# Optimization experiments

Measured on AMD Instinct MI355X. Metric: run time of the kernel, lower is better.

## Reference

```python
import jax, jax.numpy as jnp
import numpy as np

N, V, J, NB = 512, 3889, 35, 20
PARENTS = np.array([0, 0, 1, 2, 3, 4, 5, 6, 7, 8, 9, 6, 11, 12, 13, 6, 15, 16, 17, 18,
                    16, 20, 21, 22, 23, 16, 25, 26, 27, 28, 29, 30, 16, 1, 1], dtype=np.int32)


def _rodrigues(theta):
    # theta: [M,3] axis-angle -> [M,3,3] rotation matrices (batch_rodrigues)
    angle = jnp.sqrt(jnp.sum(theta * theta, axis=1, keepdims=True) + 1e-8)  # [M,1]
    r = theta / angle                                                        # [M,3]
    c = jnp.cos(angle)[..., None]                                            # [M,1,1]
    s = jnp.sin(angle)[..., None]
    rr = r[:, :, None] * r[:, None, :]                                       # [M,3,3]
    z = jnp.zeros_like(r[:, 0])
    K = jnp.stack([z, -r[:, 2], r[:, 1],
                   r[:, 2], z, -r[:, 0],
                   -r[:, 1], r[:, 0], z], axis=1).reshape(-1, 3, 3)
    eye = jnp.eye(3, dtype=theta.dtype)
    return c * eye + (1.0 - c) * rr + s * K


def _make_A(R, t):
    # R: [N,3,3], t: [N,3] -> homogeneous [N,4,4]
    n = R.shape[0]
    top = jnp.concatenate([R, t[:, :, None]], axis=2)                        # [N,3,4]
    bot = jnp.broadcast_to(jnp.array([0.0, 0.0, 0.0, 1.0], R.dtype), (n, 1, 4))
    return jnp.concatenate([top, bot], axis=1)


def _global_rigid(Rs, Jp, scales, parents):
    # Rs: [N,35,3,3], Jp: [N,35,3], scales: [N,35,3] (diag scale factors)
    # diag(s_par)^-1 @ R @ diag(s) == R * s[col] / s_par[row]
    results = [_make_A(Rs[:, 0], Jp[:, 0])]
    for i in range(1, len(parents)):  # fixed 35-joint kinematic tree
        p = int(parents[i])
        j_here = Jp[:, i] - Jp[:, p]
        rot_new = Rs[:, i] * (scales[:, i][:, None, :] / scales[:, p][:, :, None])
        results.append(results[p] @ _make_A(rot_new, j_here))
    results = jnp.stack(results, axis=1)                                     # [N,35,4,4]
    new_J = results[:, :, :3, 3]
    # A = results - pad(results @ [J;0]) : subtract rest-pose bone from last column
    init_bone = jnp.einsum('njab,njb->nja', results[:, :, :, :3], Jp)        # [N,35,4]
    A = results - jnp.pad(init_bone[..., None], ((0, 0), (0, 0), (0, 0), (3, 0)))
    return new_J, A


def reference(beta, theta, betas_extra, deform_verts, trans, v_template,
              shapedirs, posedirs, J_regressor, weights, parents):
    par = np.asarray(jax.device_get(parents))
    n = beta.shape[0]
    v_shaped = v_template + deform_verts + (beta @ shapedirs).reshape(n, V, 3)
    Jp = jnp.einsum('nvc,vj->njc', v_shaped, J_regressor)                    # [N,35,3]
    Rs = _rodrigues(theta.reshape(n * J, 3)).reshape(n, J, 3, 3)
    pose_feature = (Rs[:, 1:] - jnp.eye(3, dtype=Rs.dtype)).reshape(n, 306)
    v_posed = (pose_feature @ posedirs).reshape(n, V, 3) + v_shaped
    scales = betas_extra.reshape(n, J, 3)
    _, A = _global_rigid(Rs, Jp, scales, par)
    T = jnp.einsum('vj,njab->nvab', weights, A)                              # [N,V,4,4] LBS blend
    v_h = jnp.concatenate([v_posed, jnp.ones((n, V, 1), v_posed.dtype)], axis=2)
    verts = jnp.einsum('nvab,nvb->nva', T, v_h)[..., :3] + trans[:, None, :]
    joints = jnp.einsum('nvc,vj->njc', verts, J_regressor)
    return verts, joints, Rs


def setup_inputs() -> dict:
    key = jax.random.key(0)
    ks = jax.random.split(key, 10)
    beta = 0.5 * jax.random.normal(ks[0], (N, NB), jnp.float32)
    theta = 0.2 * jax.random.normal(ks[1], (N, J * 3), jnp.float32)
    betas_extra = jnp.exp(0.1 * jax.random.normal(ks[2], (N, J * 3), jnp.float32))  # positive scales ~1
    deform_verts = 0.01 * jax.random.normal(ks[3], (N, V, 3), jnp.float32)
    trans = jax.random.normal(ks[4], (N, 3), jnp.float32)
    v_template = jax.random.normal(ks[5], (V, 3), jnp.float32)
    shapedirs = 0.01 * jax.random.normal(ks[6], (NB, V * 3), jnp.float32)
    posedirs = 0.01 * jax.random.normal(ks[7], (306, V * 3), jnp.float32)
    Jr = jax.random.uniform(ks[8], (V, J), jnp.float32)
    J_regressor = Jr / jnp.sum(Jr, axis=0, keepdims=True)   # columns sum to 1
    Wt = jax.random.uniform(ks[9], (V, J), jnp.float32)
    weights = Wt / jnp.sum(Wt, axis=1, keepdims=True)       # rows sum to 1 (skinning weights)
    return {"beta": beta, "theta": theta, "betas_extra": betas_extra,
            "deform_verts": deform_verts, "trans": trans, "v_template": v_template,
            "shapedirs": shapedirs, "posedirs": posedirs, "J_regressor": J_regressor,
            "weights": weights, "parents": jnp.asarray(PARENTS)}
```

## Files before the change

### kernel.cpp

```cpp
#include <hip/hip_runtime.h>

#define N_   512
#define V_   3889
#define V3   11667
#define J_   35
#define NB_  20
#define PF_K 306
#define KP2  352
#define KS2  11
#define EP2  11776
#define WROWS 3920
#define VP   3904
#define JRROWS 36

typedef __attribute__((ext_vector_type(8))) short short8;
typedef __attribute__((ext_vector_type(4))) float f32x4;

__constant__ int c_parents[J_] = {0,0,1,2,3,4,5,6,7,8,9,6,11,12,13,6,15,16,17,18,
                                  16,20,21,22,23,16,25,26,27,28,29,30,16,1,1};

static __device__ __forceinline__ unsigned short f2bf(float x) {
  union { float f; unsigned int u; } v; v.f = x;
  unsigned int r = v.u + 0x7FFF + ((v.u >> 16) & 1);
  return (unsigned short)(r >> 16);
}

#define PA_JRT 549
#define PA_WTS 245
#define PA_PD  2024
#define PA_BLOCKS (PA_JRT + PA_WTS + PA_PD)
__global__ __launch_bounds__(256) void k_prep_a(
    const float* __restrict__ Jr,  const float* __restrict__ wts,
    const float* __restrict__ pd,  const float* __restrict__ sd,
    float* __restrict__ JrT, unsigned short* __restrict__ wtsB,
    unsigned short* __restrict__ pdT) {
  int b = blockIdx.x;
  int t = threadIdx.x;
  if (b < PA_JRT) {
    int idx = b * 256 + t;
    if (idx >= JRROWS * VP) return;
    int j = idx / VP, v = idx - j * VP;
    JrT[idx] = (j < J_ && v < V_) ? Jr[v * J_ + j] : 0.f;
  } else if (b < PA_JRT + PA_WTS) {
    int bb = b - PA_JRT;
    int v   = bb * 16 + (t >> 4);
    int jk0 = (t & 15) * 4;
    unsigned short pk[4];
#pragma unroll
    for (int i = 0; i < 4; ++i) {
      int j = jk0 + i;
      float x = (v < V_ && j < J_) ? wts[(size_t)v * J_ + j] : 0.f;
      pk[i] = f2bf(x);
    }
    *(unsigned long long*)(wtsB + (size_t)v * 64 + jk0) = *(unsigned long long*)pk;
  } else {
    int pp = b - (PA_JRT + PA_WTS);
    int ec = pp % 184, o4 = pp / 184;
    int e  = ec * 64 + (t & 63);
    int oc = o4 * 4 + (t >> 6);
    int k0 = oc * 8;
    bool ev = e < V3;
    union { unsigned short u[8]; short8 s; } pk;
#pragma unroll
    for (int ii = 0; ii < 8; ++ii) {
      int k = k0 + ii;
      float x = 0.f;
      if (ev && k < PF_K)            x = pd[(size_t)k * V3 + e];
      else if (ev && k < PF_K + NB_) x = sd[(size_t)(k - PF_K) * V3 + e];
      pk.u[ii] = f2bf(x);
    }
    *(short8*)(pdT + (size_t)e * KP2 + k0) = pk.s;
  }
}

#define JRJG 9
__global__ __launch_bounds__(512) void k_jp_plus(
    const float* __restrict__ deform, const float* __restrict__ JrT,
    const float* __restrict__ vt,     const float* __restrict__ sd,
    float* __restrict__ JpRaw, float* __restrict__ vtsdJr) {
  __shared__ float part[8][27];
  int b = blockIdx.x;
  int t = threadIdx.x;
  int lane = t & 63, w = t >> 6;
  int jg = w & 3, vh = w >> 2;
  int j0 = jg * JRJG;

  const float* s0;
  int c0, cn;
  bool tail;
  if (b < N_) {
    s0 = deform + (size_t)b * V3;
    c0 = vh ? 8 : 0; cn = vh ? 7 : 8; tail = (vh == 1);
  } else {
    int bb = b - N_;
    int d = bb >> 2, ch = bb & 3;
    s0 = (d == 0) ? vt : sd + (size_t)(d - 1) * V3;
    c0 = ch * 4 + vh * 2; cn = 2; tail = false;
    if (ch == 3 && vh == 1) { cn = 1; tail = true; }
  }

  const float* jrb = JrT + (size_t)j0 * VP;
  float acc[JRJG][3];
#pragma unroll
  for (int jj = 0; jj < JRJG; ++jj)
#pragma unroll
    for (int cc = 0; cc < 3; ++cc) acc[jj][cc] = 0.f;

  for (int i = 0; i < cn; ++i) {
    int v = (c0 + i) * 256 + lane * 4;
    f32x4 jr4[JRJG];
#pragma unroll
    for (int jj = 0; jj < JRJG; ++jj)
      jr4[jj] = *(const f32x4*)&jrb[(size_t)jj * VP + v];
    const float* dp = s0 + 3 * v;
    f32x4 da = *(const f32x4*)(dp);
    f32x4 db = *(const f32x4*)(dp + 4);
    f32x4 dc = *(const f32x4*)(dp + 8);
#pragma unroll
    for (int jj = 0; jj < JRJG; ++jj) {
      acc[jj][0] += jr4[jj][0]*da[0] + jr4[jj][1]*da[3] + jr4[jj][2]*db[2] + jr4[jj][3]*dc[1];
      acc[jj][1] += jr4[jj][0]*da[1] + jr4[jj][1]*db[0] + jr4[jj][2]*db[3] + jr4[jj][3]*dc[2];
      acc[jj][2] += jr4[jj][0]*da[2] + jr4[jj][1]*db[1] + jr4[jj][2]*dc[0] + jr4[jj][3]*dc[3];
    }
  }

  if (tail) {
    int v = 15 * 256 + lane * 4;
#pragma unroll
    for (int k = 0; k < 4; ++k) {
      int vv = v + k;
      if (vv < V_) {
        float dx = s0[3*vv], dy = s0[3*vv+1], dz = s0[3*vv+2];
#pragma unroll
        for (int jj = 0; jj < JRJG; ++jj) {
          float jr = jrb[(size_t)jj * VP + vv];
          acc[jj][0] += jr * dx; acc[jj][1] += jr * dy; acc[jj][2] += jr * dz;
        }
      }
    }
  }

#pragma unroll
  for (int jj = 0; jj < JRJG; ++jj)
#pragma unroll
    for (int cc = 0; cc < 3; ++cc) {
      float v = acc[jj][cc];
#pragma unroll
      for (int off = 32; off > 0; off >>= 1)
        v += __shfl_down(v, off, 64);
      if (lane == 0) part[w][jj * 3 + cc] = v;
    }
  __syncthreads();

  if (t < 108) {
    int g = t / 27, idx = t % 27;
    int j = g * JRJG + idx / 3;
    if (j < J_) {
      float val = part[g][idx] + part[g + 4][idx];
      if (b < N_) JpRaw[b * 105 + j * 3 + idx % 3] = val;
      else atomicAdd(&vtsdJr[((b - N_) >> 2) * 105 + j * 3 + idx % 3], val);
    }
  }
}

__global__ __launch_bounds__(512) void k_jreduce5(
    const float* __restrict__ src, const float* __restrict__ JrT,
    float* __restrict__ dst) {
  __shared__ float part[8][27];
  int t = threadIdx.x;
  int lane = t & 63;
  int w = t >> 6;
  int jg = w & 3, vh = w >> 2;
  int n = blockIdx.x;
  int j0 = jg * JRJG;
  const float* s0 = src + (size_t)n * V3;
  const float* jrb = JrT + (size_t)j0 * VP;

  int c0 = vh ? 8 : 0;
  int cn = vh ? 7 : 8;
  bool tail = (vh == 1);

  float acc[JRJG][3];
#pragma unroll
  for (int jj = 0; jj < JRJG; ++jj)
#pragma unroll
    for (int cc = 0; cc < 3; ++cc) acc[jj][cc] = 0.f;

  for (int i = 0; i < cn; ++i) {
    int v = (c0 + i) * 256 + lane * 4;
    f32x4 jr4[JRJG];
#pragma unroll
    for (int jj = 0; jj < JRJG; ++jj)
      jr4[jj] = *(const f32x4*)&jrb[(size_t)jj * VP + v];
    const float* dp = s0 + 3 * v;
    f32x4 da = *(const f32x4*)(dp);
    f32x4 db = *(const f32x4*)(dp + 4);
    f32x4 dc = *(const f32x4*)(dp + 8);
#pragma unroll
    for (int jj = 0; jj < JRJG; ++jj) {
      acc[jj][0] += jr4[jj][0]*da[0] + jr4[jj][1]*da[3] + jr4[jj][2]*db[2] + jr4[jj][3]*dc[1];
      acc[jj][1] += jr4[jj][0]*da[1] + jr4[jj][1]*db[0] + jr4[jj][2]*db[3] + jr4[jj][3]*dc[2];
      acc[jj][2] += jr4[jj][0]*da[2] + jr4[jj][1]*db[1] + jr4[jj][2]*dc[0] + jr4[jj][3]*dc[3];
    }
  }

  if (tail) {
    int v = 15 * 256 + lane * 4;
#pragma unroll
    for (int k = 0; k < 4; ++k) {
      int vv = v + k;
      if (vv < V_) {
        float dx = s0[3*vv], dy = s0[3*vv+1], dz = s0[3*vv+2];
#pragma unroll
        for (int jj = 0; jj < JRJG; ++jj) {
          float jr = jrb[(size_t)jj * VP + vv];
          acc[jj][0] += jr * dx; acc[jj][1] += jr * dy; acc[jj][2] += jr * dz;
        }
      }
    }
  }

#pragma unroll
  for (int jj = 0; jj < JRJG; ++jj)
#pragma unroll
    for (int cc = 0; cc < 3; ++cc) {
      float v = acc[jj][cc];
#pragma unroll
      for (int off = 32; off > 0; off >>= 1)
        v += __shfl_down(v, off, 64);
      if (lane == 0) part[w][jj * 3 + cc] = v;
    }
  __syncthreads();

  if (t < 108) {
    int g = t / 27, idx = t % 27;
    int j = g * JRJG + idx / 3;
    if (j < J_)
      dst[n * 105 + j * 3 + idx % 3] = part[g][idx] + part[g + 4][idx];
  }
}

__global__ __launch_bounds__(256) void k_chain_rod(
    const float* __restrict__ theta, const float* __restrict__ JpRaw,
    const float* __restrict__ vtsdJr,
    const float* __restrict__ se,    const float* __restrict__ trans,
    const float* __restrict__ beta,
    float* __restrict__ Rs_out, unsigned short* __restrict__ pfA,
    unsigned short* __restrict__ AwB) {
  __shared__ float loc[4][J_][12];
  __shared__ float res[4][J_][12];
  __shared__ float Jp_s[4][J_][3];
  int t = threadIdx.x;
  int w = t >> 6, l = t & 63;
  int n = blockIdx.x * 4 + w;
  int mt = n >> 4, m = n & 15;

  float r[9];
  if (l < J_) {
    int j = l;
    const float* th = theta + n * (J_ * 3) + j * 3;
    float t0 = th[0], t1 = th[1], t2 = th[2];
    float angle = sqrtf(t0 * t0 + t1 * t1 + t2 * t2 + 1e-8f);
    float inv = 1.0f / angle;
    float r0 = t0 * inv, r1 = t1 * inv, r2 = t2 * inv;
    float s, c;
    sincosf(angle, &s, &c);
    float omc = 1.0f - c;
    r[0] = c + omc * r0 * r0;      r[1] = omc * r0 * r1 - s * r2;  r[2] = omc * r0 * r2 + s * r1;
    r[3] = omc * r1 * r0 + s * r2; r[4] = c + omc * r1 * r1;       r[5] = omc * r1 * r2 - s * r0;
    r[6] = omc * r2 * r0 - s * r1; r[7] = omc * r2 * r1 + s * r0;  r[8] = c + omc * r2 * r2;

    float* ro = Rs_out + (size_t)n * (J_ * 9) + j * 9;
#pragma unroll
    for (int k = 0; k < 9; ++k) ro[k] = r[k];
    if (j > 0) {
#pragma unroll
      for (int kk = 0; kk < 9; ++kk) {
        int k = (j - 1) * 9 + kk;
        float v = r[kk] - ((kk == 0 || kk == 4 || kk == 8) ? 1.0f : 0.0f);
        size_t idx = ((((size_t)mt * KS2 + (k >> 5)) * 4 + ((k >> 3) & 3)) * 16 + m) * 8 + (k & 7);
        pfA[idx] = f2bf(v);
      }
    }
    const float* bn = beta + n * NB_;
#pragma unroll
    for (int cc = 0; cc < 3; ++cc) {
      int jc = j * 3 + cc;
      float val = JpRaw[n * 105 + jc] + vtsdJr[jc];
#pragma unroll
      for (int bb = 0; bb < NB_; ++bb)
        val += bn[bb] * vtsdJr[(1 + bb) * 105 + jc];
      Jp_s[w][j][cc] = val;
    }
  } else {
    unsigned short* An = AwB + (size_t)n * 16 * 64 + l;
#pragma unroll
    for (int d = 0; d < 16; ++d) An[d * 64] = 0;
    if (l < 55) {
      int k = PF_K + (l - 35);
      size_t idx = ((((size_t)mt * KS2 + (k >> 5)) * 4 + ((k >> 3) & 3)) * 16 + m) * 8 + (k & 7);
      pfA[idx] = f2bf(beta[n * NB_ + (l - 35)]);
    } else {
      for (int k = PF_K + NB_ + (l - 55); k < KP2; k += 9) {
        size_t idx = ((((size_t)mt * KS2 + (k >> 5)) * 4 + ((k >> 3) & 3)) * 16 + m) * 8 + (k & 7);
        pfA[idx] = 0;
      }
    }
  }
  __syncthreads();

  if (l < J_) {
    int j = l;
    if (j == 0) {
#pragma unroll
      for (int rr = 0; rr < 3; ++rr) {
        loc[w][0][rr * 4 + 0] = r[rr * 3 + 0];
        loc[w][0][rr * 4 + 1] = r[rr * 3 + 1];
        loc[w][0][rr * 4 + 2] = r[rr * 3 + 2];
        loc[w][0][rr * 4 + 3] = Jp_s[w][0][rr];
      }
#pragma unroll
      for (int k = 0; k < 12; ++k) res[w][0][k] = loc[w][0][k];
    } else {
      int p = c_parents[j];
      float si[3], sp[3], jh[3];
#pragma unroll
      for (int cidx = 0; cidx < 3; ++cidx) {
        si[cidx] = se[n * 105 + j * 3 + cidx];
        sp[cidx] = se[n * 105 + p * 3 + cidx];
        jh[cidx] = Jp_s[w][j][cidx] - Jp_s[w][p][cidx];
      }
#pragma unroll
      for (int rr = 0; rr < 3; ++rr) {
        float invp = 1.0f / sp[rr];
        loc[w][j][rr * 4 + 0] = r[rr * 3 + 0] * si[0] * invp;
        loc[w][j][rr * 4 + 1] = r[rr * 3 + 1] * si[1] * invp;
        loc[w][j][rr * 4 + 2] = r[rr * 3 + 2] * si[2] * invp;
        loc[w][j][rr * 4 + 3] = jh[rr];
      }
    }
  }
  __syncthreads();

  for (int i = 1; i < J_; ++i) {
    if (l < 12) {
      int p = c_parents[i];
      int rr = l >> 2, cc = l & 3;
      float acc = (cc == 3) ? res[w][p][rr * 4 + 3] : 0.f;
#pragma unroll
      for (int k = 0; k < 3; ++k)
        acc += res[w][p][rr * 4 + k] * loc[w][i][k * 4 + cc];
      res[w][i][l] = acc;
    }
    __syncthreads();
  }

  if (l < J_) {
    int j = l;
    float jx = Jp_s[w][j][0];
    float jy = Jp_s[w][j][1];
    float jz = Jp_s[w][j][2];
    unsigned short* An = AwB + (size_t)n * 16 * 64 + j;
#pragma unroll
    for (int rr = 0; rr < 3; ++rr) {
      float a0 = res[w][j][rr * 4 + 0];
      float a1 = res[w][j][rr * 4 + 1];
      float a2 = res[w][j][rr * 4 + 2];
      float a3 = res[w][j][rr * 4 + 3] - (a0 * jx + a1 * jy + a2 * jz)
               + trans[n * 3 + rr];
      An[(rr * 4 + 0) * 64] = f2bf(a0);
      An[(rr * 4 + 1) * 64] = f2bf(a1);
      An[(rr * 4 + 2) * 64] = f2bf(a2);
      An[(rr * 4 + 3) * 64] = f2bf(a3);
    }
  }
}

#define LSTR 242
__global__ __launch_bounds__(256) void k_vposed_skin(
    const unsigned short* __restrict__ pfA, const unsigned short* __restrict__ pdT,
    const unsigned short* __restrict__ AwB, const unsigned short* __restrict__ wtsB,
    const float* __restrict__ vt, const float* __restrict__ deform,
    float* __restrict__ verts) {
  __shared__ float lds[64 * LSTR];
  int t = threadIdx.x;
  int wv = t >> 6, lane = t & 63;
  int q = lane >> 4, col = lane & 15;
  int bx = blockIdx.x, by = blockIdx.y;
  int mtg0 = by * 4;
  int ebase = bx * 240 + wv * 64;

  const short8* Ap = (const short8*)pfA;
  const short8* Bp = (const short8*)pdT;

  f32x4 acc[4][4];
#pragma unroll
  for (int mt = 0; mt < 4; ++mt)
#pragma unroll
    for (int et = 0; et < 4; ++et) acc[mt][et] = (f32x4){0.f, 0.f, 0.f, 0.f};

#pragma unroll
  for (int ks = 0; ks < KS2; ++ks) {
    short8 a[4];
#pragma unroll
    for (int mt = 0; mt < 4; ++mt)
      a[mt] = Ap[(((mtg0 + mt) * KS2 + ks) * 4 + q) * 16 + col];
    short8 b[4];
#pragma unroll
    for (int et = 0; et < 4; ++et)
      b[et] = Bp[(size_t)(ebase + et * 16 + col) * (KP2 / 8) + ks * 4 + q];
#pragma unroll
    for (int mt = 0; mt < 4; ++mt)
#pragma unroll
      for (int et = 0; et < 4; ++et)
        acc[mt][et] = __builtin_amdgcn_mfma_f32_16x16x32_bf16(a[mt], b[et], acc[mt][et], 0, 0, 0);
  }

#pragma unroll
  for (int et = 0; et < 4; ++et) {
    int e_loc = wv * 64 + et * 16 + col;
    int e = bx * 240 + e_loc;
    bool ev = (e < V3) && (e_loc < 240);
    float vte = ev ? vt[e] : 0.f;
#pragma unroll
    for (int mt = 0; mt < 4; ++mt) {
#pragma unroll
      for (int r = 0; r < 4; ++r) {
        int n_loc = mt * 16 + q * 4 + r;
        if (ev) {
          int n = by * 64 + n_loc;
          float df = deform[(size_t)n * V3 + e];
          lds[n_loc * LSTR + e_loc] = acc[mt][et][r] + vte + df;
        }
      }
    }
  }
  __syncthreads();

  short8 bw0[5], bw1[5];
#pragma unroll
  for (int v5 = 0; v5 < 5; ++v5) {
    int v = bx * 80 + v5 * 16 + col;
    const short8* Wp = (const short8*)(wtsB + (size_t)v * 64);
    bw0[v5] = Wp[q];
    bw1[v5] = Wp[4 + q];
  }
#pragma unroll 2
  for (int ni = 0; ni < 16; ++ni) {
    int n_loc = wv * 16 + ni;
    int n = by * 64 + n_loc;
    const short8* Aq = (const short8*)(AwB + ((size_t)n * 16 + col) * 64);
    short8 a0 = Aq[q];
    short8 a1 = Aq[4 + q];
#pragma unroll
    for (int v5 = 0; v5 < 5; ++v5) {
      f32x4 s = (f32x4){0.f, 0.f, 0.f, 0.f};
      s = __builtin_amdgcn_mfma_f32_16x16x32_bf16(a0, bw0[v5], s, 0, 0, 0);
      s = __builtin_amdgcn_mfma_f32_16x16x32_bf16(a1, bw1[v5], s, 0, 0, 0);
      int vl = v5 * 16 + col;
      int v = bx * 80 + vl;
      if (v < V_ && q < 3) {
        float x = lds[n_loc * LSTR + 3 * vl + 0];
        float y = lds[n_loc * LSTR + 3 * vl + 1];
        float z = lds[n_loc * LSTR + 3 * vl + 2];
        verts[(size_t)n * V3 + 3 * v + q] = s[0] * x + s[1] * y + s[2] * z + s[3];
      }
    }
  }
}

extern "C" void kernel_launch(void* const* d_in, const int* in_sizes, int n_in,
                              void* d_out, int out_size, void* d_ws, size_t ws_size,
                              hipStream_t stream) {
  const float* beta   = (const float*)d_in[0];
  const float* theta  = (const float*)d_in[1];
  const float* se     = (const float*)d_in[2];
  const float* deform = (const float*)d_in[3];
  const float* trans  = (const float*)d_in[4];
  const float* vt     = (const float*)d_in[5];
  const float* sd     = (const float*)d_in[6];
  const float* pd     = (const float*)d_in[7];
  const float* Jr     = (const float*)d_in[8];
  const float* wts    = (const float*)d_in[9];

  float* out    = (float*)d_out;
  float* verts  = out;
  float* joints = out + (size_t)N_ * V3;
  float* Rs     = joints + (size_t)N_ * 105;

  char* w = (char*)d_ws;
  unsigned short* pdT    = (unsigned short*)w;
  unsigned short* pfA    = (unsigned short*)(w + 8290304);
  float* JpRaw  = (float*)(w + 8650752);
  unsigned short* AwB    = (unsigned short*)(w + 8865792);
  float* JrT    = (float*)(w + 9914368);
  unsigned short* wtsB   = (unsigned short*)(w + 10476544);
  float* vtsdJr = (float*)(w + 10978304);

  hipMemsetAsync(vtsdJr, 0, 21 * 105 * sizeof(float), stream);
  k_prep_a<<<PA_BLOCKS, 256, 0, stream>>>(Jr, wts, pd, sd, JrT, wtsB, pdT);
  k_jp_plus<<<N_ + 84, 512, 0, stream>>>(deform, JrT, vt, sd, JpRaw, vtsdJr);
  k_chain_rod<<<N_ / 4, 256, 0, stream>>>(theta, JpRaw, vtsdJr, se, trans, beta,
                                          Rs, pfA, AwB);
  k_vposed_skin<<<dim3(49, 8), 256, 0, stream>>>(pfA, pdT, AwB, wtsB, vt, deform, verts);
  k_jreduce5<<<N_, 512, 0, stream>>>(verts, JrT, joints);
}
```

Measured before the change: 209.4 us.

## Process four batch items per block in joint-regressor reductions to reuse JrT loads

Both joint-regression kernels now handle four batch samples per block instead of one, loading each J_regressor tile once and applying it to four deform or vertex rows. This cuts repeated JrT global and L2 traffic by a factor of four and shrinks the grid from 512 to 128 blocks. The cost is four times more accumulator registers per thread (108 floats), which can lower occupancy or cause spills, and fewer blocks may underfill the 256 CUs.

```diff
diff --git a/kernel.cpp b/kernel.cpp
--- a/kernel.cpp
+++ b/kernel.cpp
@@ -12,6 +12,7 @@
 #define WROWS 3920
 #define VP   3904
 #define JRROWS 36
+#define NBLK 128
 
 typedef __attribute__((ext_vector_type(8))) short short8;
 typedef __attribute__((ext_vector_type(4))) float f32x4;
@@ -78,165 +79,257 @@
     const float* __restrict__ deform, const float* __restrict__ JrT,
     const float* __restrict__ vt,     const float* __restrict__ sd,
     float* __restrict__ JpRaw, float* __restrict__ vtsdJr) {
-  __shared__ float part[8][27];
+  __shared__ float part[8][108];
   int b = blockIdx.x;
   int t = threadIdx.x;
   int lane = t & 63, w = t >> 6;
   int jg = w & 3, vh = w >> 2;
   int j0 = jg * JRJG;
-
-  const float* s0;
-  int c0, cn;
-  bool tail;
-  if (b < N_) {
-    s0 = deform + (size_t)b * V3;
-    c0 = vh ? 8 : 0; cn = vh ? 7 : 8; tail = (vh == 1);
+  const float* jrb = JrT + (size_t)j0 * VP;
+
+  if (b < NBLK) {
+    int n0 = b * 4;
+    float acc[4][JRJG][3];
+#pragma unroll
+    for (int nn = 0; nn < 4; ++nn)
+#pragma unroll
+      for (int jj = 0; jj < JRJG; ++jj)
+#pragma unroll
+        for (int cc = 0; cc < 3; ++cc) acc[nn][jj][cc] = 0.f;
+
+    int c0 = vh ? 8 : 0;
+    int cn = vh ? 7 : 8;
+    for (int i = 0; i < cn; ++i) {
+      int v = (c0 + i) * 256 + lane * 4;
+      f32x4 jr4[JRJG];
+#pragma unroll
+      for (int jj = 0; jj < JRJG; ++jj)
+        jr4[jj] = *(const f32x4*)&jrb[(size_t)jj * VP + v];
+#pragma unroll
+      for (int nn = 0; nn < 4; ++nn) {
+        const float* dp = deform + (size_t)(n0 + nn) * V3 + 3 * v;
+        f32x4 da = *(const f32x4*)(dp);
+        f32x4 db = *(const f32x4*)(dp + 4);
+        f32x4 dc = *(const f32x4*)(dp + 8);
+#pragma unroll
+        for (int jj = 0; jj < JRJG; ++jj) {
+          acc[nn][jj][0] += jr4[jj][0]*da[0] + jr4[jj][1]*da[3] + jr4[jj][2]*db[2] + jr4[jj][3]*dc[1];
+          acc[nn][jj][1] += jr4[jj][0]*da[1] + jr4[jj][1]*db[0] + jr4[jj][2]*db[3] + jr4[jj][3]*dc[2];
+          acc[nn][jj][2] += jr4[jj][0]*da[2] + jr4[jj][1]*db[1] + jr4[jj][2]*dc[0] + jr4[jj][3]*dc[3];
+        }
+      }
+    }
+
+    if (vh == 1) {
+      int v = 15 * 256 + lane * 4;
+#pragma unroll
+      for (int k = 0; k < 4; ++k) {
+        int vv = v + k;
+        if (vv < V_) {
+          float jr[JRJG];
+#pragma unroll
+          for (int jj = 0; jj < JRJG; ++jj)
+            jr[jj] = jrb[(size_t)jj * VP + vv];
+#pragma unroll
+          for (int nn = 0; nn < 4; ++nn) {
+            const float* dp = deform + (size_t)(n0 + nn) * V3 + 3 * vv;
+            float dx = dp[0], dy = dp[1], dz = dp[2];
+#pragma unroll
+            for (int jj = 0; jj < JRJG; ++jj) {
+              acc[nn][jj][0] += jr[jj] * dx;
+              acc[nn][jj][1] += jr[jj] * dy;
+              acc[nn][jj][2] += jr[jj] * dz;
+            }
+          }
+        }
+      }
+    }
+
+#pragma unroll
+    for (int nn = 0; nn < 4; ++nn)
+#pragma unroll
+      for (int jj = 0; jj < JRJG; ++jj)
+#pragma unroll
+        for (int cc = 0; cc < 3; ++cc) {
+          float v = acc[nn][jj][cc];
+#pragma unroll
+          for (int off = 32; off > 0; off >>= 1)
+            v += __shfl_down(v, off, 64);
+          if (lane == 0) part[w][nn * 27 + jj * 3 + cc] = v;
+        }
+    __syncthreads();
+
+    if (t < 108) {
+      int g = t / 27, idx = t % 27;
+      int j = g * JRJG + idx / 3;
+      if (j < J_) {
+#pragma unroll
+        for (int nn = 0; nn < 4; ++nn)
+          JpRaw[(n0 + nn) * 105 + j * 3 + idx % 3] =
+              part[g][nn * 27 + idx] + part[g + 4][nn * 27 + idx];
+      }
+    }
   } else {
-    int bb = b - N_;
+    int bb = b - NBLK;
     int d = bb >> 2, ch = bb & 3;
-    s0 = (d == 0) ? vt : sd + (size_t)(d - 1) * V3;
-    c0 = ch * 4 + vh * 2; cn = 2; tail = false;
+    const float* s0 = (d == 0) ? vt : sd + (size_t)(d - 1) * V3;
+    int c0 = ch * 4 + vh * 2, cn = 2;
+    bool tail = false;
     if (ch == 3 && vh == 1) { cn = 1; tail = true; }
-  }
-
+
+    float acc[JRJG][3];
+#pragma unroll
+    for (int jj = 0; jj < JRJG; ++jj)
+#pragma unroll
+      for (int cc = 0; cc < 3; ++cc) acc[jj][cc] = 0.f;
+
+    for (int i = 0; i < cn; ++i) {
+      int v = (c0 + i) * 256 + lane * 4;
+      f32x4 jr4[JRJG];
+#pragma unroll
+      for (int jj = 0; jj < JRJG; ++jj)
+        jr4[jj] = *(const f32x4*)&jrb[(size_t)jj * VP + v];
+      const float* dp = s0 + 3 * v;
+      f32x4 da = *(const f32x4*)(dp);
+      f32x4 db = *(const f32x4*)(dp + 4);
+      f32x4 dc = *(const f32x4*)(dp + 8);
+#pragma unroll
+      for (int jj = 0; jj < JRJG; ++jj) {
+        acc[jj][0] += jr4[jj][0]*da[0] + jr4[jj][1]*da[3] + jr4[jj][2]*db[2] + jr4[jj][3]*dc[1];
+        acc[jj][1] += jr4[jj][0]*da[1] + jr4[jj][1]*db[0] + jr4[jj][2]*db[3] + jr4[jj][3]*dc[2];
+        acc[jj][2] += jr4[jj][0]*da[2] + jr4[jj][1]*db[1] + jr4[jj][2]*dc[0] + jr4[jj][3]*dc[3];
+      }
+    }
+
+    if (tail) {
+      int v = 15 * 256 + lane * 4;
+#pragma unroll
+      for (int k = 0; k < 4; ++k) {
+        int vv = v + k;
+        if (vv < V_) {
+          float dx = s0[3*vv], dy = s0[3*vv+1], dz = s0[3*vv+2];
+#pragma unroll
+          for (int jj = 0; jj < JRJG; ++jj) {
+            float jr = jrb[(size_t)jj * VP + vv];
+            acc[jj][0] += jr * dx; acc[jj][1] += jr * dy; acc[jj][2] += jr * dz;
+          }
+        }
+      }
+    }
+
+#pragma unroll
+    for (int jj = 0; jj < JRJG; ++jj)
+#pragma unroll
+      for (int cc = 0; cc < 3; ++cc) {
+        float v = acc[jj][cc];
+#pragma unroll
+        for (int off = 32; off > 0; off >>= 1)
+          v += __shfl_down(v, off, 64);
+        if (lane == 0) part[w][jj * 3 + cc] = v;
+      }
+    __syncthreads();
+
+    if (t < 108) {
+      int g = t / 27, idx = t % 27;
+      int j = g * JRJG + idx / 3;
+      if (j < J_)
+        atomicAdd(&vtsdJr[(bb >> 2) * 105 + j * 3 + idx % 3],
+                  part[g][idx] + part[g + 4][idx]);
+    }
+  }
+}
+
+__global__ __launch_bounds__(512) void k_jreduce5(
+    const float* __restrict__ src, const float* __restrict__ JrT,
+    float* __restrict__ dst) {
+  __shared__ float part[8][108];
+  int t = threadIdx.x;
+  int lane = t & 63;
+  int w = t >> 6;
+  int jg = w & 3, vh = w >> 2;
+  int n0 = blockIdx.x * 4;
+  int j0 = jg * JRJG;
   const float* jrb = JrT + (size_t)j0 * VP;
-  float acc[JRJG][3];
-#pragma unroll
-  for (int jj = 0; jj < JRJG; ++jj)
-#pragma unroll
-    for (int cc = 0; cc < 3; ++cc) acc[jj][cc] = 0.f;
-
+
+  float acc[4][JRJG][3];
+#pragma unroll
+  for (int nn = 0; nn < 4; ++nn)
+#pragma unroll
+    for (int jj = 0; jj < JRJG; ++jj)
+#pragma unroll
+      for (int cc = 0; cc < 3; ++cc) acc[nn][jj][cc] = 0.f;
+
+  int c0 = vh ? 8 : 0;
+  int cn = vh ? 7 : 8;
   for (int i = 0; i < cn; ++i) {
     int v = (c0 + i) * 256 + lane * 4;
     f32x4 jr4[JRJG];
 #pragma unroll
     for (int jj = 0; jj < JRJG; ++jj)
       jr4[jj] = *(const f32x4*)&jrb[(size_t)jj * VP + v];
-    const float* dp = s0 + 3 * v;
-    f32x4 da = *(const f32x4*)(dp);
-    f32x4 db = *(const f32x4*)(dp + 4);
-    f32x4 dc = *(const f32x4*)(dp + 8);
-#pragma unroll
-    for (int jj = 0; jj < JRJG; ++jj) {
-      acc[jj][0] += jr4[jj][0]*da[0] + jr4[jj][1]*da[3] + jr4[jj][2]*db[2] + jr4[jj][3]*dc[1];
-      acc[jj][1] += jr4[jj][0]*da[1] + jr4[jj][1]*db[0] + jr4[jj][2]*db[3] + jr4[jj][3]*dc[2];
-      acc[jj][2] += jr4[jj][0]*da[2] + jr4[jj][1]*db[1] + jr4[jj][2]*dc[0] + jr4[jj][3]*dc[3];
-    }
-  }
-
-  if (tail) {
+#pragma unroll
+    for (int nn = 0; nn < 4; ++nn) {
+      const float* dp = src + (size_t)(n0 + nn) * V3 + 3 * v;
+      f32x4 da = *(const f32x4*)(dp);
+      f32x4 db = *(const f32x4*)(dp + 4);
+      f32x4 dc = *(const f32x4*)(dp + 8);
+#pragma unroll
+      for (int jj = 0; jj < JRJG; ++jj) {
+        acc[nn][jj][0] += jr4[jj][0]*da[0] + jr4[jj][1]*da[3] + jr4[jj][2]*db[2] + jr4[jj][3]*dc[1];
+        acc[nn][jj][1] += jr4[jj][0]*da[1] + jr4[jj][1]*db[0] + jr4[jj][2]*db[3] + jr4[jj][3]*dc[2];
+        acc[nn][jj][2] += jr4[jj][0]*da[2] + jr4[jj][1]*db[1] + jr4[jj][2]*dc[0] + jr4[jj][3]*dc[3];
+      }
+    }
+  }
+
+  if (vh == 1) {
     int v = 15 * 256 + lane * 4;
 #pragma unroll
     for (int k = 0; k < 4; ++k) {
       int vv = v + k;
       if (vv < V_) {
-        float dx = s0[3*vv], dy = s0[3*vv+1], dz = s0[3*vv+2];
-#pragma unroll
-        for (int jj = 0; jj < JRJG; ++jj) {
-          float jr = jrb[(size_t)jj * VP + vv];
-          acc[jj][0] += jr * dx; acc[jj][1] += jr * dy; acc[jj][2] += jr * dz;
+        float jr[JRJG];
+#pragma unroll
+        for (int jj = 0; jj < JRJG; ++jj)
+          jr[jj] = jrb[(size_t)jj * VP + vv];
+#pragma unroll
+        for (int nn = 0; nn < 4; ++nn) {
+          const float* dp = src + (size_t)(n0 + nn) * V3 + 3 * vv;
+          float dx = dp[0], dy = dp[1], dz = dp[2];
+#pragma unroll
+          for (int jj = 0; jj < JRJG; ++jj) {
+            acc[nn][jj][0] += jr[jj] * dx;
+            acc[nn][jj][1] += jr[jj] * dy;
+            acc[nn][jj][2] += jr[jj] * dz;
+          }
         }
       }
     }
   }
 
 #pragma unroll
-  for (int jj = 0; jj < JRJG; ++jj)
-#pragma unroll
-    for (int cc = 0; cc < 3; ++cc) {
-      float v = acc[jj][cc];
-#pragma unroll
-      for (int off = 32; off > 0; off >>= 1)
-        v += __shfl_down(v, off, 64);
-      if (lane == 0) part[w][jj * 3 + cc] = v;
-    }
+  for (int nn = 0; nn < 4; ++nn)
+#pragma unroll
+    for (int jj = 0; jj < JRJG; ++jj)
+#pragma unroll
+      for (int cc = 0; cc < 3; ++cc) {
+        float v = acc[nn][jj][cc];
+#pragma unroll
+        for (int off = 32; off > 0; off >>= 1)
+          v += __shfl_down(v, off, 64);
+        if (lane == 0) part[w][nn * 27 + jj * 3 + cc] = v;
+      }
   __syncthreads();
 
   if (t < 108) {
     int g = t / 27, idx = t % 27;
     int j = g * JRJG + idx / 3;
     if (j < J_) {
-      float val = part[g][idx] + part[g + 4][idx];
-      if (b < N_) JpRaw[b * 105 + j * 3 + idx % 3] = val;
-      else atomicAdd(&vtsdJr[((b - N_) >> 2) * 105 + j * 3 + idx % 3], val);
-    }
-  }
-}
-
-__global__ __launch_bounds__(512) void k_jreduce5(
-    const float* __restrict__ src, const float* __restrict__ JrT,
-    float* __restrict__ dst) {
-  __shared__ float part[8][27];
-  int t = threadIdx.x;
-  int lane = t & 63;
-  int w = t >> 6;
-  int jg = w & 3, vh = w >> 2;
-  int n = blockIdx.x;
-  int j0 = jg * JRJG;
-  const float* s0 = src + (size_t)n * V3;
-  const float* jrb = JrT + (size_t)j0 * VP;
-
-  int c0 = vh ? 8 : 0;
-  int cn = vh ? 7 : 8;
-  bool tail = (vh == 1);
-
-  float acc[JRJG][3];
-#pragma unroll
-  for (int jj = 0; jj < JRJG; ++jj)
-#pragma unroll
-    for (int cc = 0; cc < 3; ++cc) acc[jj][cc] = 0.f;
-
-  for (int i = 0; i < cn; ++i) {
-    int v = (c0 + i) * 256 + lane * 4;
-    f32x4 jr4[JRJG];
-#pragma unroll
-    for (int jj = 0; jj < JRJG; ++jj)
-      jr4[jj] = *(const f32x4*)&jrb[(size_t)jj * VP + v];
-    const float* dp = s0 + 3 * v;
-    f32x4 da = *(const f32x4*)(dp);
-    f32x4 db = *(const f32x4*)(dp + 4);
-    f32x4 dc = *(const f32x4*)(dp + 8);
-#pragma unroll
-    for (int jj = 0; jj < JRJG; ++jj) {
-      acc[jj][0] += jr4[jj][0]*da[0] + jr4[jj][1]*da[3] + jr4[jj][2]*db[2] + jr4[jj][3]*dc[1];
-      acc[jj][1] += jr4[jj][0]*da[1] + jr4[jj][1]*db[0] + jr4[jj][2]*db[3] + jr4[jj][3]*dc[2];
-      acc[jj][2] += jr4[jj][0]*da[2] + jr4[jj][1]*db[1] + jr4[jj][2]*dc[0] + jr4[jj][3]*dc[3];
-    }
-  }
-
-  if (tail) {
-    int v = 15 * 256 + lane * 4;
-#pragma unroll
-    for (int k = 0; k < 4; ++k) {
-      int vv = v + k;
-      if (vv < V_) {
-        float dx = s0[3*vv], dy = s0[3*vv+1], dz = s0[3*vv+2];
-#pragma unroll
-        for (int jj = 0; jj < JRJG; ++jj) {
-          float jr = jrb[(size_t)jj * VP + vv];
-          acc[jj][0] += jr * dx; acc[jj][1] += jr * dy; acc[jj][2] += jr * dz;
-        }
-      }
-    }
-  }
-
-#pragma unroll
-  for (int jj = 0; jj < JRJG; ++jj)
-#pragma unroll
-    for (int cc = 0; cc < 3; ++cc) {
-      float v = acc[jj][cc];
-#pragma unroll
-      for (int off = 32; off > 0; off >>= 1)
-        v += __shfl_down(v, off, 64);
-      if (lane == 0) part[w][jj * 3 + cc] = v;
-    }
-  __syncthreads();
-
-  if (t < 108) {
-    int g = t / 27, idx = t % 27;
-    int j = g * JRJG + idx / 3;
-    if (j < J_)
-      dst[n * 105 + j * 3 + idx % 3] = part[g][idx] + part[g + 4][idx];
+#pragma unroll
+      for (int nn = 0; nn < 4; ++nn)
+        dst[(n0 + nn) * 105 + j * 3 + idx % 3] =
+            part[g][nn * 27 + idx] + part[g + 4][nn * 27 + idx];
+    }
   }
 }
 
@@ -499,9 +592,9 @@
 
   hipMemsetAsync(vtsdJr, 0, 21 * 105 * sizeof(float), stream);
   k_prep_a<<<PA_BLOCKS, 256, 0, stream>>>(Jr, wts, pd, sd, JrT, wtsB, pdT);
-  k_jp_plus<<<N_ + 84, 512, 0, stream>>>(deform, JrT, vt, sd, JpRaw, vtsdJr);
+  k_jp_plus<<<NBLK + 84, 512, 0, stream>>>(deform, JrT, vt, sd, JpRaw, vtsdJr);
   k_chain_rod<<<N_ / 4, 256, 0, stream>>>(theta, JpRaw, vtsdJr, se, trans, beta,
                                           Rs, pfA, AwB);
   k_vposed_skin<<<dim3(49, 8), 256, 0, stream>>>(pfA, pdT, AwB, wtsB, vt, deform, verts);
-  k_jreduce5<<<N_, 512, 0, stream>>>(verts, JrT, joints);
+  k_jreduce5<<<NBLK, 512, 0, stream>>>(verts, JrT, joints);
 }
```

Result: slower. 256.5 us (+22.5%).

## Replace FP32 joint-regressor reductions with bf16 MFMA GEMM over expanded regressor

Applied to the files above, without the earlier changes.

Builds a bf16 expanded joint regressor (105 x 11776, zero-padded per coordinate) in the prep kernel. Both per-batch joint regressions, over deform and over the final verts, now run as split-K 16x16x32 bf16 MFMA GEMMs that write partial planes. The planes are summed in chain_rod and in a new fold kernel. This trades the scalar FP32 dot-product kernels for matrix cores, at the cost of bf16 rounding of vertices, extra planes traffic, more prep work and one more launch.

```diff
diff --git a/kernel.cpp b/kernel.cpp
--- a/kernel.cpp
+++ b/kernel.cpp
@@ -9,9 +9,12 @@
 #define KP2  352
 #define KS2  11
 #define EP2  11776
-#define WROWS 3920
 #define VP   3904
 #define JRROWS 36
+#define JCP  112
+#define KB_  23
+#define ECH  512
+#define PLN  57344
 
 typedef __attribute__((ext_vector_type(8))) short short8;
 typedef __attribute__((ext_vector_type(4))) float f32x4;
@@ -28,12 +31,13 @@
 #define PA_JRT 549
 #define PA_WTS 245
 #define PA_PD  2024
-#define PA_BLOCKS (PA_JRT + PA_WTS + PA_PD)
+#define PA_JB  644
+#define PA_BLOCKS (PA_JRT + PA_WTS + PA_PD + PA_JB)
 __global__ __launch_bounds__(256) void k_prep_a(
     const float* __restrict__ Jr,  const float* __restrict__ wts,
     const float* __restrict__ pd,  const float* __restrict__ sd,
     float* __restrict__ JrT, unsigned short* __restrict__ wtsB,
-    unsigned short* __restrict__ pdT) {
+    unsigned short* __restrict__ pdT, unsigned short* __restrict__ JrBigT) {
   int b = blockIdx.x;
   int t = threadIdx.x;
   if (b < PA_JRT) {
@@ -53,7 +57,7 @@
       pk[i] = f2bf(x);
     }
     *(unsigned long long*)(wtsB + (size_t)v * 64 + jk0) = *(unsigned long long*)pk;
-  } else {
+  } else if (b < PA_JRT + PA_WTS + PA_PD) {
     int pp = b - (PA_JRT + PA_WTS);
     int ec = pp % 184, o4 = pp / 184;
     int e  = ec * 64 + (t & 63);
@@ -70,36 +74,41 @@
       pk.u[ii] = f2bf(x);
     }
     *(short8*)(pdT + (size_t)e * KP2 + k0) = pk.s;
+  } else {
+    int o = (b - (PA_JRT + PA_WTS + PA_PD)) * 256 + t;
+    int jc = o / 1472;
+    int eo = (o - jc * 1472) * 8;
+    int jj = jc / 3, cc = jc - jj * 3;
+    union { unsigned short u[8]; short8 s; } pk;
+#pragma unroll
+    for (int i = 0; i < 8; ++i) {
+      int e = eo + i;
+      int v = e / 3, ce = e - v * 3;
+      float x = (jc < 105 && e < V3 && ce == cc) ? Jr[v * J_ + jj] : 0.f;
+      pk.u[i] = f2bf(x);
+    }
+    *(short8*)(JrBigT + (size_t)jc * EP2 + eo) = pk.s;
   }
 }
 
 #define JRJG 9
-__global__ __launch_bounds__(512) void k_jp_plus(
-    const float* __restrict__ deform, const float* __restrict__ JrT,
-    const float* __restrict__ vt,     const float* __restrict__ sd,
-    float* __restrict__ JpRaw, float* __restrict__ vtsdJr) {
+__global__ __launch_bounds__(512) void k_jp84(
+    const float* __restrict__ JrT, const float* __restrict__ vt,
+    const float* __restrict__ sd,  float* __restrict__ vtsdJr) {
   __shared__ float part[8][27];
   int b = blockIdx.x;
   int t = threadIdx.x;
   int lane = t & 63, w = t >> 6;
   int jg = w & 3, vh = w >> 2;
   int j0 = jg * JRJG;
-
-  const float* s0;
-  int c0, cn;
-  bool tail;
-  if (b < N_) {
-    s0 = deform + (size_t)b * V3;
-    c0 = vh ? 8 : 0; cn = vh ? 7 : 8; tail = (vh == 1);
-  } else {
-    int bb = b - N_;
-    int d = bb >> 2, ch = bb & 3;
-    s0 = (d == 0) ? vt : sd + (size_t)(d - 1) * V3;
-    c0 = ch * 4 + vh * 2; cn = 2; tail = false;
-    if (ch == 3 && vh == 1) { cn = 1; tail = true; }
-  }
-
   const float* jrb = JrT + (size_t)j0 * VP;
+
+  int d = b >> 2, ch = b & 3;
+  const float* s0 = (d == 0) ? vt : sd + (size_t)(d - 1) * V3;
+  int c0 = ch * 4 + vh * 2, cn = 2;
+  bool tail = false;
+  if (ch == 3 && vh == 1) { cn = 1; tail = true; }
+
   float acc[JRJG][3];
 #pragma unroll
   for (int jj = 0; jj < JRJG; ++jj)
@@ -155,93 +164,81 @@
   if (t < 108) {
     int g = t / 27, idx = t % 27;
     int j = g * JRJG + idx / 3;
-    if (j < J_) {
-      float val = part[g][idx] + part[g + 4][idx];
-      if (b < N_) JpRaw[b * 105 + j * 3 + idx % 3] = val;
-      else atomicAdd(&vtsdJr[((b - N_) >> 2) * 105 + j * 3 + idx % 3], val);
-    }
-  }
-}
-
-__global__ __launch_bounds__(512) void k_jreduce5(
-    const float* __restrict__ src, const float* __restrict__ JrT,
-    float* __restrict__ dst) {
-  __shared__ float part[8][27];
-  int t = threadIdx.x;
-  int lane = t & 63;
-  int w = t >> 6;
-  int jg = w & 3, vh = w >> 2;
-  int n = blockIdx.x;
-  int j0 = jg * JRJG;
-  const float* s0 = src + (size_t)n * V3;
-  const float* jrb = JrT + (size_t)j0 * VP;
-
-  int c0 = vh ? 8 : 0;
-  int cn = vh ? 7 : 8;
-  bool tail = (vh == 1);
-
-  float acc[JRJG][3];
-#pragma unroll
-  for (int jj = 0; jj < JRJG; ++jj)
-#pragma unroll
-    for (int cc = 0; cc < 3; ++cc) acc[jj][cc] = 0.f;
-
-  for (int i = 0; i < cn; ++i) {
-    int v = (c0 + i) * 256 + lane * 4;
-    f32x4 jr4[JRJG];
-#pragma unroll
-    for (int jj = 0; jj < JRJG; ++jj)
-      jr4[jj] = *(const f32x4*)&jrb[(size_t)jj * VP + v];
-    const float* dp = s0 + 3 * v;
-    f32x4 da = *(const f32x4*)(dp);
-    f32x4 db = *(const f32x4*)(dp + 4);
-    f32x4 dc = *(const f32x4*)(dp + 8);
-#pragma unroll
-    for (int jj = 0; jj < JRJG; ++jj) {
-      acc[jj][0] += jr4[jj][0]*da[0] + jr4[jj][1]*da[3] + jr4[jj][2]*db[2] + jr4[jj][3]*dc[1];
-      acc[jj][1] += jr4[jj][0]*da[1] + jr4[jj][1]*db[0] + jr4[jj][2]*db[3] + jr4[jj][3]*dc[2];
-      acc[jj][2] += jr4[jj][0]*da[2] + jr4[jj][1]*db[1] + jr4[jj][2]*dc[0] + jr4[jj][3]*dc[3];
-    }
-  }
-
-  if (tail) {
-    int v = 15 * 256 + lane * 4;
-#pragma unroll
-    for (int k = 0; k < 4; ++k) {
-      int vv = v + k;
-      if (vv < V_) {
-        float dx = s0[3*vv], dy = s0[3*vv+1], dz = s0[3*vv+2];
-#pragma unroll
-        for (int jj = 0; jj < JRJG; ++jj) {
-          float jr = jrb[(size_t)jj * VP + vv];
-          acc[jj][0] += jr * dx; acc[jj][1] += jr * dy; acc[jj][2] += jr * dz;
-        }
-      }
-    }
-  }
-
-#pragma unroll
-  for (int jj = 0; jj < JRJG; ++jj)
-#pragma unroll
-    for (int cc = 0; cc < 3; ++cc) {
-      float v = acc[jj][cc];
-#pragma unroll
-      for (int off = 32; off > 0; off >>= 1)
-        v += __shfl_down(v, off, 64);
-      if (lane == 0) part[w][jj * 3 + cc] = v;
-    }
-  __syncthreads();
-
-  if (t < 108) {
-    int g = t / 27, idx = t % 27;
-    int j = g * JRJG + idx / 3;
     if (j < J_)
-      dst[n * 105 + j * 3 + idx % 3] = part[g][idx] + part[g + 4][idx];
-  }
+      atomicAdd(&vtsdJr[(b >> 2) * 105 + j * 3 + idx % 3],
+                part[g][idx] + part[g + 4][idx]);
+  }
+}
+
+__global__ __launch_bounds__(64) void k_jrgemm(
+    const float* __restrict__ X, const unsigned short* __restrict__ JrBigT,
+    float* __restrict__ planes) {
+  int lane = threadIdx.x;
+  int q = lane >> 4, c = lane & 15;
+  int n = blockIdx.x * 16 + c;
+  int kb = blockIdx.y;
+  int e0 = kb * ECH;
+  const float* xr = X + (size_t)n * V3;
+  const short8* Ap = (const short8*)JrBigT;
+
+  f32x4 acc[7];
+#pragma unroll
+  for (int tt = 0; tt < 7; ++tt) acc[tt] = (f32x4){0.f, 0.f, 0.f, 0.f};
+
+  bool safe = (e0 + ECH <= V3);
+  if (safe) {
+#pragma unroll
+    for (int ks = 0; ks < ECH / 32; ++ks) {
+      int eb = e0 + ks * 32 + q * 8;
+      f32x4 x0 = *(const f32x4*)(xr + eb);
+      f32x4 x1 = *(const f32x4*)(xr + eb + 4);
+      union { unsigned short u[8]; short8 s; } bq;
+#pragma unroll
+      for (int i = 0; i < 4; ++i) { bq.u[i] = f2bf(x0[i]); bq.u[4 + i] = f2bf(x1[i]); }
+#pragma unroll
+      for (int tt = 0; tt < 7; ++tt) {
+        short8 a = Ap[((size_t)(tt * 16 + c) * EP2 + eb) >> 3];
+        acc[tt] = __builtin_amdgcn_mfma_f32_16x16x32_bf16(a, bq.s, acc[tt], 0, 0, 0);
+      }
+    }
+  } else {
+#pragma unroll
+    for (int ks = 0; ks < ECH / 32; ++ks) {
+      int eb = e0 + ks * 32 + q * 8;
+      union { unsigned short u[8]; short8 s; } bq;
+#pragma unroll
+      for (int i = 0; i < 8; ++i) {
+        int e = eb + i;
+        float x = (e < V3) ? xr[e] : 0.f;
+        bq.u[i] = f2bf(x);
+      }
+#pragma unroll
+      for (int tt = 0; tt < 7; ++tt) {
+        short8 a = Ap[((size_t)(tt * 16 + c) * EP2 + eb) >> 3];
+        acc[tt] = __builtin_amdgcn_mfma_f32_16x16x32_bf16(a, bq.s, acc[tt], 0, 0, 0);
+      }
+    }
+  }
+
+  float* pl = planes + (size_t)kb * PLN + (size_t)n * JCP;
+#pragma unroll
+  for (int tt = 0; tt < 7; ++tt)
+    *(f32x4*)(pl + tt * 16 + q * 4) = acc[tt];
+}
+
+__global__ __launch_bounds__(256) void k_fold_joints(
+    const float* __restrict__ planes, float* __restrict__ joints) {
+  int g = blockIdx.x * 256 + threadIdx.x;
+  int n = g / 105, jc = g - n * 105;
+  float s = 0.f;
+#pragma unroll
+  for (int kb = 0; kb < KB_; ++kb)
+    s += planes[(size_t)kb * PLN + n * JCP + jc];
+  joints[g] = s;
 }
 
 __global__ __launch_bounds__(256) void k_chain_rod(
-    const float* __restrict__ theta, const float* __restrict__ JpRaw,
+    const float* __restrict__ theta, const float* __restrict__ planes,
     const float* __restrict__ vtsdJr,
     const float* __restrict__ se,    const float* __restrict__ trans,
     const float* __restrict__ beta,
@@ -286,7 +283,10 @@
 #pragma unroll
     for (int cc = 0; cc < 3; ++cc) {
       int jc = j * 3 + cc;
-      float val = JpRaw[n * 105 + jc] + vtsdJr[jc];
+      float val = vtsdJr[jc];
+#pragma unroll
+      for (int kb = 0; kb < KB_; ++kb)
+        val += planes[(size_t)kb * PLN + n * JCP + jc];
 #pragma unroll
       for (int bb = 0; bb < NB_; ++bb)
         val += bn[bb] * vtsdJr[(1 + bb) * 105 + jc];
@@ -491,17 +491,20 @@
   char* w = (char*)d_ws;
   unsigned short* pdT    = (unsigned short*)w;
   unsigned short* pfA    = (unsigned short*)(w + 8290304);
-  float* JpRaw  = (float*)(w + 8650752);
-  unsigned short* AwB    = (unsigned short*)(w + 8865792);
-  float* JrT    = (float*)(w + 9914368);
-  unsigned short* wtsB   = (unsigned short*)(w + 10476544);
-  float* vtsdJr = (float*)(w + 10978304);
+  float* planes = (float*)(w + 8650752);
+  unsigned short* AwB    = (unsigned short*)(w + 13926400);
+  float* JrT    = (float*)(w + 14974976);
+  unsigned short* wtsB   = (unsigned short*)(w + 15537152);
+  unsigned short* JrBigT = (unsigned short*)(w + 16038912);
+  float* vtsdJr = (float*)(w + 18676736);
 
   hipMemsetAsync(vtsdJr, 0, 21 * 105 * sizeof(float), stream);
-  k_prep_a<<<PA_BLOCKS, 256, 0, stream>>>(Jr, wts, pd, sd, JrT, wtsB, pdT);
-  k_jp_plus<<<N_ + 84, 512, 0, stream>>>(deform, JrT, vt, sd, JpRaw, vtsdJr);
-  k_chain_rod<<<N_ / 4, 256, 0, stream>>>(theta, JpRaw, vtsdJr, se, trans, beta,
+  k_prep_a<<<PA_BLOCKS, 256, 0, stream>>>(Jr, wts, pd, sd, JrT, wtsB, pdT, JrBigT);
+  k_jp84<<<84, 512, 0, stream>>>(JrT, vt, sd, vtsdJr);
+  k_jrgemm<<<dim3(32, KB_), 64, 0, stream>>>(deform, JrBigT, planes);
+  k_chain_rod<<<N_ / 4, 256, 0, stream>>>(theta, planes, vtsdJr, se, trans, beta,
                                           Rs, pfA, AwB);
   k_vposed_skin<<<dim3(49, 8), 256, 0, stream>>>(pfA, pdT, AwB, wtsB, vt, deform, verts);
-  k_jreduce5<<<N_, 512, 0, stream>>>(verts, JrT, joints);
-}
+  k_jrgemm<<<dim3(32, KB_), 64, 0, stream>>>(verts, JrBigT, planes);
+  k_fold_joints<<<210, 256, 0, stream>>>(planes, joints);
+}
```

After: 217.7 us. 1.04x slower.
